# Optimization experiments

Hardware: AMD Instinct MI355X
Metric: run time of the kernel (lower is better)

Reference implementation:

```python
import jax, jax.numpy as jnp
import numpy as np
import math

V, D, H, F, L = 32000, 1024, 16, 4096, 6
B, S_DEC, S_ENC = 8, 512, 512
EPS = 1e-5


def _pos_encoding(seq_len, d_model):
    pos = jnp.arange(seq_len, dtype=jnp.float32)[:, None]
    div = jnp.exp(jnp.arange(0, d_model, 2, dtype=jnp.float32) * (-math.log(10000.0) / d_model))
    pe = jnp.zeros((seq_len, d_model), dtype=jnp.float32)
    pe = pe.at[:, 0::2].set(jnp.sin(pos * div))
    pe = pe.at[:, 1::2].set(jnp.cos(pos * div))
    return pe


def _layernorm(x, g, b):
    m = jnp.mean(x, axis=-1, keepdims=True)
    v = jnp.mean((x - m) ** 2, axis=-1, keepdims=True)
    return (x - m) * jax.lax.rsqrt(v + EPS) * g + b


def _mha(q_in, k_in, v_in, w, b, mask, n_heads):
    # w: [4, D, D] stored as [in, out] (q,k,v,o); b: [4, D]
    bsz, sq, dm = q_in.shape
    hd = dm // n_heads
    q = (q_in @ w[0] + b[0]).reshape(bsz, sq, n_heads, hd)
    k = (k_in @ w[1] + b[1]).reshape(bsz, -1, n_heads, hd)
    v = (v_in @ w[2] + b[2]).reshape(bsz, -1, n_heads, hd)
    scores = jnp.einsum('bqhd,bkhd->bhqk', q, k) / jnp.sqrt(jnp.asarray(hd, q.dtype))
    if mask is not None:
        scores = jnp.where(mask, jnp.asarray(-1e15, scores.dtype), scores)
    att = jax.nn.softmax(scores, axis=-1)
    out = jnp.einsum('bhqk,bkhd->bqhd', att, v).reshape(bsz, sq, dm)
    return out @ w[3] + b[3]


def setup_inputs() -> dict:
    key = jax.random.key(0)
    ks = jax.random.split(key, 16)
    sc = 0.02
    enc_out = jax.random.normal(ks[0], (B, S_ENC, D), dtype=jnp.float32)
    dec_in = jax.random.randint(ks[1], (B, S_DEC), 0, V, dtype=jnp.int64)
    # no padding on encoder side
    enc_dec_mask = jnp.zeros((1, 1, S_DEC, S_ENC), dtype=bool)
    # causal mask: True above the diagonal -> masked out
    fut_mask = jnp.triu(jnp.ones((S_DEC, S_DEC), dtype=bool), k=1)[None, None]
    return {
        'encoder_output': enc_out,
        'decoder_input': dec_in,
        'encoder_decoder_mask': enc_dec_mask,
        'decoder_future_mask': fut_mask,
        'embed_table': jax.random.normal(ks[2], (V, D), dtype=jnp.float32) * sc,
        'sa_w': jax.random.normal(ks[3], (L, 4, D, D), dtype=jnp.float32) * sc,
        'sa_b': jnp.zeros((L, 4, D), dtype=jnp.float32),
        'ca_w': jax.random.normal(ks[4], (L, 4, D, D), dtype=jnp.float32) * sc,
        'ca_b': jnp.zeros((L, 4, D), dtype=jnp.float32),
        'ffn_w1': jax.random.normal(ks[5], (L, D, F), dtype=jnp.float32) * sc,
        'ffn_b1': jnp.zeros((L, F), dtype=jnp.float32),
        'ffn_w2': jax.random.normal(ks[6], (L, F, D), dtype=jnp.float32) * sc,
        'ffn_b2': jnp.zeros((L, D), dtype=jnp.float32),
        'ln_g': jnp.ones((L, 3, D), dtype=jnp.float32),
        'ln_b': jnp.zeros((L, 3, D), dtype=jnp.float32),
        'final_g': jnp.ones((D,), dtype=jnp.float32),
        'final_b': jnp.zeros((D,), dtype=jnp.float32),
    }


def reference(encoder_output, decoder_input, encoder_decoder_mask, decoder_future_mask,
              embed_table, sa_w, sa_b, ca_w, ca_b, ffn_w1, ffn_b1, ffn_w2, ffn_b2,
              ln_g, ln_b, final_g, final_b):
    seq_len = decoder_input.shape[1]
    x = embed_table[decoder_input] * jnp.asarray(math.sqrt(D), jnp.float32)
    x = x + _pos_encoding(seq_len, D)
    for l in range(L):
        # pre-norm self-attention (dropout is identity at eval)
        h = _layernorm(x, ln_g[l, 0], ln_b[l, 0])
        x = x + _mha(h, h, h, sa_w[l], sa_b[l], decoder_future_mask, H)
        # pre-norm cross-attention
        h = _layernorm(x, ln_g[l, 1], ln_b[l, 1])
        x = x + _mha(h, encoder_output, encoder_output, ca_w[l], ca_b[l], encoder_decoder_mask, H)
        # pre-norm FFN
        h = _layernorm(x, ln_g[l, 2], ln_b[l, 2])
        x = x + jax.nn.relu(h @ ffn_w1[l] + ffn_b1[l]) @ ffn_w2[l] + ffn_b2[l]
    return _layernorm(x, final_g, final_b)
```

## Files before the change

### kernel.cpp

```cpp
#include <hip/hip_runtime.h>
#include <hip/hip_bf16.h>

typedef __attribute__((ext_vector_type(8))) short bf16x8;
typedef __attribute__((ext_vector_type(4))) float f32x4;
typedef __hip_bfloat16 bf16;

constexpr int DM   = 1024;
constexpr int NH   = 16;
constexpr int HD   = 64;
constexpr int FF   = 4096;
constexpr int NL   = 6;
constexpr int NB_  = 8;
constexpr int SEQL = 512;
constexpr int NTOK = NB_ * SEQL;

__device__ __forceinline__ void gl_lds16(const void* g, void* l) {
  __builtin_amdgcn_global_load_lds(
      (const __attribute__((address_space(1))) unsigned int*)g,
      (__attribute__((address_space(3))) unsigned int*)l, 16, 0, 0);
}

__global__ __launch_bounds__(256) void transpose_cvt(const float* __restrict__ src,
                                                     bf16* __restrict__ dst,
                                                     int R, int C) {
  __shared__ float tile[32][33];
  size_t mo = (size_t)blockIdx.z * R * C;
  src += mo; dst += mo;
  int c0 = blockIdx.x * 32, r0 = blockIdx.y * 32;
  int tx = threadIdx.x, ty = threadIdx.y;
  #pragma unroll
  for (int j = 0; j < 4; ++j)
    tile[ty + 8*j][tx] = src[(size_t)(r0 + ty + 8*j) * C + c0 + tx];
  __syncthreads();
  #pragma unroll
  for (int j = 0; j < 4; ++j)
    dst[(size_t)(c0 + ty + 8*j) * R + r0 + tx] = __float2bfloat16(tile[tx][ty + 8*j]);
}

__global__ __launch_bounds__(256) void cvt_bf16(const float* __restrict__ s,
                                                bf16* __restrict__ d) {
  size_t i = (size_t)blockIdx.x * 256 + threadIdx.x;
  float4 v = ((const float4*)s)[i];
  union { bf16 h[4]; uint2 u; } t;
  t.h[0] = __float2bfloat16(v.x); t.h[1] = __float2bfloat16(v.y);
  t.h[2] = __float2bfloat16(v.z); t.h[3] = __float2bfloat16(v.w);
  *(uint2*)(d + i * 4) = t.u;
}

__global__ __launch_bounds__(256) void vtrans(const bf16* __restrict__ in,
                                              bf16* __restrict__ out) {
  __shared__ bf16 tile[32][33];
  int t0 = blockIdx.x * 32, d0 = blockIdx.y * 32;
  int tx = threadIdx.x, ty = threadIdx.y;
  #pragma unroll
  for (int j = 0; j < 4; ++j)
    tile[ty + 8*j][tx] = in[(size_t)(t0 + ty + 8*j) * 3072 + 2048 + d0 + tx];
  __syncthreads();
  #pragma unroll
  for (int j = 0; j < 4; ++j)
    out[(size_t)(d0 + ty + 8*j) * NTOK + t0 + tx] = tile[tx][ty + 8*j];
}

__global__ __launch_bounds__(256) void embed_pe(const int* __restrict__ tok,
                                                const float* __restrict__ table,
                                                float* __restrict__ x) {
  int t = blockIdx.x;
  int s = t & (SEQL - 1);
  int tk = tok[t];
  int d = threadIdx.x * 4;
  float4 e = *(const float4*)(table + (size_t)tk * DM + d);
  float o[4] = {e.x, e.y, e.z, e.w};
  const float NEGC = -9.210340371976184f / 1024.0f;
  #pragma unroll
  for (int i = 0; i < 4; ++i) {
    int dd = d + i;
    float div = __expf((float)(dd & ~1) * NEGC);
    float arg = (float)s * div;
    float pe = (dd & 1) ? cosf(arg) : sinf(arg);
    o[i] = o[i] * 32.0f + pe;
  }
  float4 ov = {o[0], o[1], o[2], o[3]};
  *(float4*)(x + (size_t)t * DM + d) = ov;
}

__device__ __forceinline__ void ln_wave(float4 v[4], const float* __restrict__ g,
                                        const float* __restrict__ bb,
                                        int row, int lane, bf16* ob, float* of, int outf32) {
  float s = 0.0f;
  #pragma unroll
  for (int i = 0; i < 4; ++i) s += v[i].x + v[i].y + v[i].z + v[i].w;
  #pragma unroll
  for (int o = 32; o; o >>= 1) s += __shfl_xor(s, o);
  float mean = s * (1.0f / DM);
  float s2 = 0.0f;
  #pragma unroll
  for (int i = 0; i < 4; ++i) {
    v[i].x -= mean; v[i].y -= mean; v[i].z -= mean; v[i].w -= mean;
    s2 += v[i].x*v[i].x + v[i].y*v[i].y + v[i].z*v[i].z + v[i].w*v[i].w;
  }
  #pragma unroll
  for (int o = 32; o; o >>= 1) s2 += __shfl_xor(s2, o);
  float rs = rsqrtf(s2 * (1.0f / DM) + 1e-5f);
  #pragma unroll
  for (int i = 0; i < 4; ++i) {
    int c = (lane + i * 64) * 4;
    float4 gg = *(const float4*)(g + c);
    float4 bv = *(const float4*)(bb + c);
    float y0 = v[i].x * rs * gg.x + bv.x;
    float y1 = v[i].y * rs * gg.y + bv.y;
    float y2 = v[i].z * rs * gg.z + bv.z;
    float y3 = v[i].w * rs * gg.w + bv.w;
    if (outf32) {
      float4 ov = {y0, y1, y2, y3};
      *(float4*)(of + (size_t)row * DM + c) = ov;
    } else {
      union { bf16 h[4]; uint2 u; } t;
      t.h[0] = __float2bfloat16(y0); t.h[1] = __float2bfloat16(y1);
      t.h[2] = __float2bfloat16(y2); t.h[3] = __float2bfloat16(y3);
      *(uint2*)(ob + (size_t)row * DM + c) = t.u;
    }
  }
}

template<int OUTF32>
__global__ __launch_bounds__(256) void ln_kernel(const float* __restrict__ x,
                                                 const float* __restrict__ g,
                                                 const float* __restrict__ bb,
                                                 bf16* __restrict__ ob,
                                                 float* __restrict__ of) {
  int wv = threadIdx.x >> 6, lane = threadIdx.x & 63;
  int row = blockIdx.x * 4 + wv;
  const float4* xr = (const float4*)(x + (size_t)row * DM);
  float4 v[4];
  #pragma unroll
  for (int i = 0; i < 4; ++i) v[i] = xr[lane + i * 64];
  ln_wave(v, g, bb, row, lane, ob, of, OUTF32);
}

template<int OUTF32>
__global__ __launch_bounds__(256) void ln_fused4(float* __restrict__ x,
                                                 const float* __restrict__ p,
                                                 const float* __restrict__ bias,
                                                 const float* __restrict__ g,
                                                 const float* __restrict__ bb,
                                                 bf16* __restrict__ ob,
                                                 float* __restrict__ of) {
  int wv = threadIdx.x >> 6, lane = threadIdx.x & 63;
  int row = blockIdx.x * 4 + wv;
  size_t rb = (size_t)row * DM;
  const size_t NM = (size_t)NTOK * DM;
  float4 v[4];
  #pragma unroll
  for (int i = 0; i < 4; ++i) {
    int c = (lane + i * 64) * 4;
    float4 xv = *(const float4*)(x + rb + c);
    float4 a0 = *(const float4*)(p + rb + c);
    float4 a1 = *(const float4*)(p + NM + rb + c);
    float4 a2 = *(const float4*)(p + 2*NM + rb + c);
    float4 a3 = *(const float4*)(p + 3*NM + rb + c);
    float4 bv = *(const float4*)(bias + c);
    xv.x += a0.x + a1.x + a2.x + a3.x + bv.x;
    xv.y += a0.y + a1.y + a2.y + a3.y + bv.y;
    xv.z += a0.z + a1.z + a2.z + a3.z + bv.z;
    xv.w += a0.w + a1.w + a2.w + a3.w + bv.w;
    *(float4*)(x + rb + c) = xv;
    v[i] = xv;
  }
  ln_wave(v, g, bb, row, lane, ob, of, OUTF32);
}

template<int EPI>
__global__ __launch_bounds__(256) void gemm_bt(const bf16* __restrict__ A,
                                               const bf16* __restrict__ Bt,
                                               const float* __restrict__ bias,
                                               bf16* __restrict__ Cb,
                                               float* __restrict__ Cf,
                                               int M, int N, int K) {
  constexpr int BN = 64, NFR = 2;
  __shared__ bf16 As[3][128 * 32];
  __shared__ bf16 Bs[3][BN * 32];
  int tid = threadIdx.x;
  int wave = tid >> 6, lane = tid & 63;
  int l4 = lane & 15, lhi = lane >> 4;
  int wr = wave >> 1, wc = wave & 1;
  int nwg = gridDim.x * gridDim.y;
  int bid = blockIdx.y * gridDim.x + blockIdx.x;
  int cpx = nwg >> 3;
  int swz = (bid & 7) * cpx + (bid >> 3);
  int bx = swz % gridDim.x, by = swz / gridDim.x;
  int brow = by * 128, bcol = bx * BN;
  f32x4 acc[4][NFR] = {};
  int srow = lane >> 2;
  int scol = (lane & 3) * 8;
  int T = K >> 5;

  auto stage = [&](int buf, int t) {
    int k0 = t * 32;
    #pragma unroll
    for (int i = 0; i < 2; ++i) {
      int rb = i * 64 + wave * 16;
      gl_lds16(A + (size_t)(brow + rb + srow) * K + k0 + scol, &As[buf][rb * 32]);
    }
    int rb = wave * 16;
    gl_lds16(Bt + (size_t)(bcol + rb + srow) * K + k0 + scol, &Bs[buf][rb * 32]);
  };
  auto compute = [&](int buf) {
    bf16x8 af[4], bfv[NFR];
    #pragma unroll
    for (int m = 0; m < 4; ++m)
      af[m] = *(const bf16x8*)&As[buf][(wr * 64 + m * 16 + l4) * 32 + lhi * 8];
    #pragma unroll
    for (int n = 0; n < NFR; ++n)
      bfv[n] = *(const bf16x8*)&Bs[buf][(wc * 32 + n * 16 + l4) * 32 + lhi * 8];
    #pragma unroll
    for (int m = 0; m < 4; ++m)
      #pragma unroll
      for (int n = 0; n < NFR; ++n)
        acc[m][n] = __builtin_amdgcn_mfma_f32_16x16x32_bf16(af[m], bfv[n], acc[m][n], 0, 0, 0);
  };

  stage(0, 0);
  stage(1, 1);
  for (int t = 0; t < T; ++t) {
    if (t < T - 1) asm volatile("s_waitcnt vmcnt(3)" ::: "memory");
    else           asm volatile("s_waitcnt vmcnt(0)" ::: "memory");
    __builtin_amdgcn_s_barrier();
    asm volatile("" ::: "memory");
    if (t + 2 < T) stage((t + 2) % 3, t + 2);
    compute(t % 3);
  }

  #pragma unroll
  for (int m = 0; m < 4; ++m) {
    int row0 = brow + wr * 64 + m * 16 + lhi * 4;
    #pragma unroll
    for (int n = 0; n < NFR; ++n) {
      int col = bcol + wc * 32 + n * 16 + l4;
      #pragma unroll
      for (int r = 0; r < 4; ++r) {
        int row = row0 + r;
        float v = acc[m][n][r];
        if (EPI == 0) {
          v += bias[col];
          Cb[(size_t)row * N + col] = __float2bfloat16(v);
        } else {
          v += bias[col];
          size_t idx = (size_t)row * N + col;
          Cf[idx] = Cf[idx] + v;
        }
      }
    }
  }
}

template<int EPI>
__global__ __launch_bounds__(512, 2) void gemm8x(const bf16* __restrict__ A,
                                                 const bf16* __restrict__ Bt,
                                                 const float* __restrict__ bias,
                                                 bf16* __restrict__ Cb,
                                                 float* __restrict__ Cf,
                                                 int M, int N, int K) {
  __shared__ bf16 S[8][8192];
  int tid = threadIdx.x;
  int wave = tid >> 6, lane = tid & 63;
  int l4 = lane & 15, lhi = lane >> 4;
  int wr = wave >> 2, wc = wave & 3;
  int nwg = gridDim.x * gridDim.y;
  int bid = blockIdx.y * gridDim.x + blockIdx.x;
  int cpx = nwg >> 3;
  int swz = (bid & 7) * cpx + (bid >> 3);
  int bx = swz % gridDim.x, by = swz / gridDim.x;
  int brow = by * 256, bcol = bx * 256;
  f32x4 acc[8][4] = {};

  int kbase = 0, Keff = K;
  if (EPI == 4) { Keff = K >> 2; kbase = blockIdx.z * Keff; }
  int T = Keff >> 6;

  int srcRow = tid >> 3;
  int srcKb  = ((tid & 7) << 4) ^ (((tid >> 5) & 1) << 5) ^ (((tid >> 4) & 1) << 6);
  int swzr   = (((l4 >> 2) & 1) << 4) ^ (((l4 >> 1) & 1) << 5);

  auto stageA = [&](int d, int half, int kt) {
    #pragma unroll
    for (int j = 0; j < 2; ++j) {
      int r = brow + half * 128 + j * 64 + srcRow;
      if (EPI == 6) r = ((r >> 10) << 12) + 2048 + (r & 1023);
      const char* src = (const char*)(A + (size_t)r * K + kbase + kt * 64) + srcKb;
      gl_lds16(src, (char*)&S[d * 2 + half][0] + j * 8192 + wave * 1024);
    }
  };
  auto stageB = [&](int d, int half, int kt) {
    #pragma unroll
    for (int j = 0; j < 2; ++j) {
      int r = bcol + half * 128 + j * 64 + srcRow;
      if (EPI == 5) r = ((r >> 10) << 12) + 1024 + (r & 1023);
      const char* src = (const char*)(Bt + (size_t)r * K + kbase + kt * 64) + srcKb;
      gl_lds16(src, (char*)&S[4 + d * 2 + half][0] + j * 8192 + wave * 1024);
    }
  };

  stageA(0, 0, 0); stageA(0, 1, 0); stageB(0, 0, 0); stageB(0, 1, 0);

  for (int i = 0; i < T; ++i) {
    int d = i & 1, od = d ^ 1;
    asm volatile("s_waitcnt vmcnt(0)" ::: "memory");
    __builtin_amdgcn_s_barrier();
    asm volatile("" ::: "memory");
    const bf16* As_ = &S[d * 2 + wr][0];
    const bf16* Bs_ = &S[4 + d * 2 + (wc >> 1)][0];
    int rB = (wc & 1) * 64;
    bool st = (i + 1) < T;

    bf16x8 bfv[4][2];
    #pragma unroll
    for (int n = 0; n < 4; ++n) {
      int r = rB + n * 16 + l4;
      #pragma unroll
      for (int ks = 0; ks < 2; ++ks)
        bfv[n][ks] = *(const bf16x8*)&Bs_[r * 64 + ((ks * 32 + lhi * 8) ^ swzr)];
    }
    bf16x8 afA[2][2], afB[2][2];
    #pragma unroll
    for (int mm = 0; mm < 2; ++mm) {
      int r = (0 * 2 + mm) * 16 + l4;
      #pragma unroll
      for (int ks = 0; ks < 2; ++ks)
        afA[mm][ks] = *(const bf16x8*)&As_[r * 64 + ((ks * 32 + lhi * 8) ^ swzr)];
    }
    if (st) { stageA(od, 0, i + 1); stageA(od, 1, i + 1); }

    #pragma unroll
    for (int mm = 0; mm < 2; ++mm) {
      int r = (1 * 2 + mm) * 16 + l4;
      #pragma unroll
      for (int ks = 0; ks < 2; ++ks)
        afB[mm][ks] = *(const bf16x8*)&As_[r * 64 + ((ks * 32 + lhi * 8) ^ swzr)];
    }
    if (st) { stageB(od, 0, i + 1); stageB(od, 1, i + 1); }
    __builtin_amdgcn_s_setprio(1);
    #pragma unroll
    for (int mm = 0; mm < 2; ++mm)
      #pragma unroll
      for (int ks = 0; ks < 2; ++ks)
        #pragma unroll
        for (int n = 0; n < 4; ++n)
          acc[0 * 2 + mm][n] = __builtin_amdgcn_mfma_f32_16x16x32_bf16(afA[mm][ks], bfv[n][ks], acc[0 * 2 + mm][n], 0, 0, 0);
    __builtin_amdgcn_s_setprio(0);

    #pragma unroll
    for (int mm = 0; mm < 2; ++mm) {
      int r = (2 * 2 + mm) * 16 + l4;
      #pragma unroll
      for (int ks = 0; ks < 2; ++ks)
        afA[mm][ks] = *(const bf16x8*)&As_[r * 64 + ((ks * 32 + lhi * 8) ^ swzr)];
    }
    __builtin_amdgcn_s_setprio(1);
    #pragma unroll
    for (int mm = 0; mm < 2; ++mm)
      #pragma unroll
      for (int ks = 0; ks < 2; ++ks)
        #pragma unroll
        for (int n = 0; n < 4; ++n)
          acc[1 * 2 + mm][n] = __builtin_amdgcn_mfma_f32_16x16x32_bf16(afB[mm][ks], bfv[n][ks], acc[1 * 2 + mm][n], 0, 0, 0);
    __builtin_amdgcn_s_setprio(0);

    #pragma unroll
    for (int mm = 0; mm < 2; ++mm) {
      int r = (3 * 2 + mm) * 16 + l4;
      #pragma unroll
      for (int ks = 0; ks < 2; ++ks)
        afB[mm][ks] = *(const bf16x8*)&As_[r * 64 + ((ks * 32 + lhi * 8) ^ swzr)];
    }
    __builtin_amdgcn_s_setprio(1);
    #pragma unroll
    for (int mm = 0; mm < 2; ++mm)
      #pragma unroll
      for (int ks = 0; ks < 2; ++ks)
        #pragma unroll
        for (int n = 0; n < 4; ++n)
          acc[2 * 2 + mm][n] = __builtin_amdgcn_mfma_f32_16x16x32_bf16(afA[mm][ks], bfv[n][ks], acc[2 * 2 + mm][n], 0, 0, 0);
    __builtin_amdgcn_s_setprio(0);

    __builtin_amdgcn_s_setprio(1);
    #pragma unroll
    for (int mm = 0; mm < 2; ++mm)
      #pragma unroll
      for (int ks = 0; ks < 2; ++ks)
        #pragma unroll
        for (int n = 0; n < 4; ++n)
          acc[3 * 2 + mm][n] = __builtin_amdgcn_mfma_f32_16x16x32_bf16(afB[mm][ks], bfv[n][ks], acc[3 * 2 + mm][n], 0, 0, 0);
    __builtin_amdgcn_s_setprio(0);
    asm volatile("" ::: "memory");
  }

  #pragma unroll
  for (int m = 0; m < 8; ++m) {
    int row0 = brow + wr * 128 + m * 16 + lhi * 4;
    #pragma unroll
    for (int n = 0; n < 4; ++n) {
      int col = bcol + wc * 64 + n * 16 + l4;
      #pragma unroll
      for (int r = 0; r < 4; ++r) {
        int row = row0 + r;
        float v = acc[m][n][r];
        if (EPI == 0) {
          v += bias[col];
          Cb[(size_t)row * N + col] = __float2bfloat16(v);
        } else if (EPI == 1) {
          v += bias[col];
          v = fmaxf(v, 0.0f);
          Cb[(size_t)row * N + col] = __float2bfloat16(v);
        } else if (EPI == 4) {
          Cf[(size_t)blockIdx.z * ((size_t)M * N) + (size_t)row * N + col] = v;
        } else if (EPI == 5) {
          v += bias[((col >> 10) << 12) + 1024 + (col & 1023)];
          Cb[(size_t)row * N + col] = __float2bfloat16(v);
        } else {
          v += bias[((row >> 10) << 12) + 2048 + (row & 1023)];
          Cb[(size_t)row * N + col] = __float2bfloat16(v);
        }
      }
    }
  }
}

template<int CAUSAL>
__global__ __launch_bounds__(256, 2) void attn_kernel(const bf16* __restrict__ qg,
                                                      const bf16* __restrict__ kg,
                                                      const bf16* __restrict__ vtg,
                                                      bf16* __restrict__ og,
                                                      int qs, int ks) {
  __shared__ bf16 P[4][16][520];
  __shared__ bf16 KV[4096];
  int qblk = blockIdx.x;
  int bh = blockIdx.y;
  int b = bh >> 4, h = bh & 15;
  int wave = threadIdx.x >> 6, lane = threadIdx.x & 63;
  int l4 = lane & 15, lhi = lane >> 4;
  int qbase = qblk * 64 + wave * 16;
  const int qmax = CAUSAL ? (qbase + 15) : 0x7fffffff;
  const int tmaxb = CAUSAL ? qblk : 7;

  int srow8 = lane >> 3;
  int sbyte = ((lane & 7) * 16) ^ (srow8 << 4);
  int rdswz = (l4 & 7) << 4;

  bf16x8 qa[2];
  {
    size_t qrow = (size_t)(b * SEQL + qbase + l4);
    #pragma unroll
    for (int kk = 0; kk < 2; ++kk)
      qa[kk] = *(const bf16x8*)&qg[qrow * qs + h * HD + kk * 32 + lhi * 8];
  }

  f32x4 acc[32] = {};
  #pragma unroll
  for (int t = 0; t < 8; ++t) {
    if (t <= tmaxb) {
      #pragma unroll
      for (int j = 0; j < 2; ++j) {
        int row = (wave * 2 + j) * 8 + srow8;
        const char* src = (const char*)(kg + (size_t)(b * SEQL + t * 64 + row) * ks + h * HD) + sbyte;
        gl_lds16(src, (char*)&KV[0] + (wave * 2 + j) * 1024);
      }
      asm volatile("s_waitcnt vmcnt(0)" ::: "memory");
      __builtin_amdgcn_s_barrier();
      asm volatile("" ::: "memory");
      #pragma unroll
      for (int n = 0; n < 4; ++n) {
        int nk = t * 4 + n;
        if (!CAUSAL || nk * 16 <= qmax) {
          #pragma unroll
          for (int kk = 0; kk < 2; ++kk) {
            bf16x8 kf = *(const bf16x8*)((const char*)&KV[0] + (n * 16 + l4) * 128 + ((kk * 64 + lhi * 16) ^ rdswz));
            acc[nk] = __builtin_amdgcn_mfma_f32_16x16x32_bf16(qa[kk], kf, acc[nk], 0, 0, 0);
          }
        }
      }
      __builtin_amdgcn_s_barrier();
      asm volatile("" ::: "memory");
    }
  }

  int qloc = qbase + lhi * 4;
  #pragma unroll
  for (int r = 0; r < 4; ++r) {
    float mx = -3.0e38f;
    #pragma unroll
    for (int n = 0; n < 32; ++n) {
      float sv = acc[n][r] * 0.125f;
      if (CAUSAL && (n * 16 + l4 > qloc + r)) sv = -3.0e38f;
      acc[n][r] = sv;
      mx = fmaxf(mx, sv);
    }
    #pragma unroll
    for (int o = 1; o < 16; o <<= 1) mx = fmaxf(mx, __shfl_xor(mx, o));
    float sum = 0.0f;
    #pragma unroll
    for (int n = 0; n < 32; ++n) {
      float p;
      if (CAUSAL && n * 16 > qmax) p = 0.0f;
      else p = __expf(acc[n][r] - mx);
      acc[n][r] = p;
      sum += p;
    }
    #pragma unroll
    for (int o = 1; o < 16; o <<= 1) sum += __shfl_xor(sum, o);
    float rcp = 1.0f / sum;
    #pragma unroll
    for (int n = 0; n < 32; ++n)
      P[wave][lhi * 4 + r][n * 16 + l4] = __float2bfloat16(acc[n][r] * rcp);
  }
  __syncthreads();

  f32x4 oacc[4] = {};
  #pragma unroll
  for (int t = 0; t < 8; ++t) {
    if (t <= tmaxb) {
      #pragma unroll
      for (int j = 0; j < 2; ++j) {
        int row = (wave * 2 + j) * 8 + srow8;
        const char* src = (const char*)(vtg + (size_t)(h * HD + row) * NTOK + b * SEQL + t * 64) + sbyte;
        gl_lds16(src, (char*)&KV[0] + (wave * 2 + j) * 1024);
      }
      asm volatile("s_waitcnt vmcnt(0)" ::: "memory");
      __builtin_amdgcn_s_barrier();
      asm volatile("" ::: "memory");
      #pragma unroll
      for (int ksl = 0; ksl < 2; ++ksl) {
        int kslot = t * 2 + ksl;
        if (!CAUSAL || kslot * 32 <= qmax) {
          bf16x8 pa = *(const bf16x8*)&P[wave][l4][kslot * 32 + lhi * 8];
          #pragma unroll
          for (int nn = 0; nn < 4; ++nn) {
            bf16x8 vf = *(const bf16x8*)((const char*)&KV[0] + (nn * 16 + l4) * 128 + ((ksl * 64 + lhi * 16) ^ rdswz));
            oacc[nn] = __builtin_amdgcn_mfma_f32_16x16x32_bf16(pa, vf, oacc[nn], 0, 0, 0);
          }
        }
      }
      __builtin_amdgcn_s_barrier();
      asm volatile("" ::: "memory");
    }
  }

  size_t orow = (size_t)(b * SEQL + qbase + lhi * 4);
  #pragma unroll
  for (int n = 0; n < 4; ++n)
    #pragma unroll
    for (int r = 0; r < 4; ++r)
      og[(orow + r) * DM + h * HD + n * 16 + l4] = __float2bfloat16(oacc[n][r]);
}

extern "C" void kernel_launch(void* const* d_in, const int* in_sizes, int n_in,
                              void* d_out, int out_size, void* d_ws, size_t ws_size,
                              hipStream_t stream) {
  (void)in_sizes; (void)n_in; (void)out_size;
  const float* enc   = (const float*)d_in[0];
  const int*   toks  = (const int*)  d_in[1];
  const float* table = (const float*)d_in[4];
  const float* sa_w  = (const float*)d_in[5];
  const float* sa_b  = (const float*)d_in[6];
  const float* ca_w  = (const float*)d_in[7];
  const float* ca_b  = (const float*)d_in[8];
  const float* f1w   = (const float*)d_in[9];
  const float* f1b   = (const float*)d_in[10];
  const float* f2w   = (const float*)d_in[11];
  const float* f2b   = (const float*)d_in[12];
  const float* lng   = (const float*)d_in[13];
  const float* lnbp  = (const float*)d_in[14];
  const float* fg    = (const float*)d_in[15];
  const float* fbp   = (const float*)d_in[16];
  float* outp = (float*)d_out;

  char* base = (char*)d_ws;
  size_t off = 0;
  auto alloc = [&](size_t nbytes) -> char* {
    char* p = base + off;
    off += (nbytes + 255) & ~(size_t)255;
    return p;
  };
  const size_t DDb = (size_t)DM * DM;
  bf16* wt_sa   = (bf16*)alloc((size_t)NL * 4 * DDb * 2);
  bf16* wt_ca   = (bf16*)alloc((size_t)NL * 4 * DDb * 2);
  bf16* wt_f1   = (bf16*)alloc((size_t)NL * FF * DM * 2);
  bf16* wt_f2   = (bf16*)alloc((size_t)NL * FF * DM * 2);
  bf16* encb    = (bf16*)alloc((size_t)NTOK * DM * 2);
  bf16* keall   = (bf16*)alloc((size_t)NTOK * NL * DM * 2);
  bf16* vteall  = (bf16*)alloc((size_t)NL * DM * NTOK * 2);
  bf16* hbuf    = (bf16*)alloc((size_t)NTOK * DM * 2);
  bf16* qkvbuf  = (bf16*)alloc((size_t)NTOK * 3 * DM * 2);
  bf16* vtbuf   = (bf16*)alloc((size_t)NTOK * DM * 2);
  bf16* aobuf   = (bf16*)alloc((size_t)NTOK * DM * 2);
  bf16* h1buf   = (bf16*)alloc((size_t)NTOK * FF * 2);
  float* xbuf   = (float*)alloc((size_t)NTOK * DM * 4);
  float* pbuf4  = (float*)alloc((size_t)4 * NTOK * DM * 4);
  if (off > ws_size) return;

  dim3 tb(32, 8);
  transpose_cvt<<<dim3(DM/32, DM/32, NL*4), tb, 0, stream>>>(sa_w, wt_sa, DM, DM);
  transpose_cvt<<<dim3(DM/32, DM/32, NL*4), tb, 0, stream>>>(ca_w, wt_ca, DM, DM);
  transpose_cvt<<<dim3(FF/32, DM/32, NL),   tb, 0, stream>>>(f1w, wt_f1, DM, FF);
  transpose_cvt<<<dim3(DM/32, FF/32, NL),   tb, 0, stream>>>(f2w, wt_f2, FF, DM);
  cvt_bf16<<<(NTOK * DM / 4) / 256, 256, 0, stream>>>(enc, encb);
  embed_pe<<<NTOK, 256, 0, stream>>>(toks, table, xbuf);

  gemm8x<5><<<dim3(NL*DM/256, NTOK/256), 512, 0, stream>>>(encb, wt_ca, ca_b, keall, nullptr, NTOK, NL*DM, DM);
  gemm8x<6><<<dim3(NTOK/256, NL*DM/256), 512, 0, stream>>>(wt_ca, encb, ca_b, vteall, nullptr, NL*DM, NTOK, DM);

  ln_kernel<0><<<NTOK/4, 256, 0, stream>>>(xbuf, lng + 0*DM, lnbp + 0*DM, hbuf, nullptr);

  for (int l = 0; l < NL; ++l) {
    const bf16* wsa = wt_sa + (size_t)l * 4 * DDb;
    const bf16* wca = wt_ca + (size_t)l * 4 * DDb;
    const float* bsa = sa_b + (size_t)l * 4 * DM;
    const float* bca = ca_b + (size_t)l * 4 * DM;
    gemm8x<0><<<dim3(3*DM/256, NTOK/256), 512, 0, stream>>>(hbuf, wsa, bsa, qkvbuf, nullptr, NTOK, 3*DM, DM);
    vtrans<<<dim3(NTOK/32, DM/32), tb, 0, stream>>>(qkvbuf, vtbuf);
    attn_kernel<1><<<dim3(SEQL/64, NB_*NH), 256, 0, stream>>>(qkvbuf, qkvbuf + DM, vtbuf, aobuf, 3*DM, 3*DM);
    gemm_bt<3><<<dim3(DM/64, NTOK/128), 256, 0, stream>>>(aobuf, wsa + 3*DDb, bsa + 3*DM, nullptr, xbuf, NTOK, DM, DM);
    ln_kernel<0><<<NTOK/4, 256, 0, stream>>>(xbuf, lng + (l*3+1)*DM, lnbp + (l*3+1)*DM, hbuf, nullptr);
    gemm_bt<0><<<dim3(DM/64, NTOK/128), 256, 0, stream>>>(hbuf, wca + 0*DDb, bca + 0*DM, qkvbuf, nullptr, NTOK, DM, DM);
    attn_kernel<0><<<dim3(SEQL/64, NB_*NH), 256, 0, stream>>>(qkvbuf, keall + l*DM, vteall + (size_t)l*DM*NTOK, aobuf, DM, NL*DM);
    gemm_bt<3><<<dim3(DM/64, NTOK/128), 256, 0, stream>>>(aobuf, wca + 3*DDb, bca + 3*DM, nullptr, xbuf, NTOK, DM, DM);
    ln_kernel<0><<<NTOK/4, 256, 0, stream>>>(xbuf, lng + (l*3+2)*DM, lnbp + (l*3+2)*DM, hbuf, nullptr);
    gemm8x<1><<<dim3(FF/256, NTOK/256), 512, 0, stream>>>(hbuf, wt_f1 + (size_t)l*FF*DM, f1b + (size_t)l*FF, h1buf, nullptr, NTOK, FF, DM);
    gemm8x<4><<<dim3(DM/256, NTOK/256, 4), 512, 0, stream>>>(h1buf, wt_f2 + (size_t)l*FF*DM, nullptr, nullptr, pbuf4, NTOK, DM, FF);
    if (l < NL - 1)
      ln_fused4<0><<<NTOK/4, 256, 0, stream>>>(xbuf, pbuf4, f2b + (size_t)l*DM,
                                               lng + ((l+1)*3+0)*DM, lnbp + ((l+1)*3+0)*DM, hbuf, nullptr);
    else
      ln_fused4<1><<<NTOK/4, 256, 0, stream>>>(xbuf, pbuf4, f2b + (size_t)l*DM,
                                               fg, fbp, nullptr, outp);
  }
}
```

Baseline: 2.028 ms.

## Merge encoder K/V GEMMs into one launch, move residual add into LN, swizzle attention grid

The two encoder-side cross-attention K and V projection GEMMs now run in a single dual-role launch, sharing one grid instead of two back-to-back kernels. The o-projection GEMMs write plain fp32 partials, and a new fused LayerNorm kernel does the residual-plus-bias add, which removes the read-modify-write of x from the GEMM epilogue. The attention grid is remapped with an XCD-style block swizzle for better cache locality. In exchange, the fused LN reads an extra fp32 buffer, and the swizzle mapping assumes a fixed grid shape.

```diff
diff --git a/kernel.cpp b/kernel.cpp
--- a/kernel.cpp
+++ b/kernel.cpp
@@ -134,6 +134,34 @@
   float4 v[4];
   #pragma unroll
   for (int i = 0; i < 4; ++i) v[i] = xr[lane + i * 64];
+  ln_wave(v, g, bb, row, lane, ob, of, OUTF32);
+}
+
+template<int OUTF32>
+__global__ __launch_bounds__(256) void ln_fused1(float* __restrict__ x,
+                                                 const float* __restrict__ p,
+                                                 const float* __restrict__ bias,
+                                                 const float* __restrict__ g,
+                                                 const float* __restrict__ bb,
+                                                 bf16* __restrict__ ob,
+                                                 float* __restrict__ of) {
+  int wv = threadIdx.x >> 6, lane = threadIdx.x & 63;
+  int row = blockIdx.x * 4 + wv;
+  size_t rb = (size_t)row * DM;
+  float4 v[4];
+  #pragma unroll
+  for (int i = 0; i < 4; ++i) {
+    int c = (lane + i * 64) * 4;
+    float4 xv = *(const float4*)(x + rb + c);
+    float4 a0 = *(const float4*)(p + rb + c);
+    float4 bv = *(const float4*)(bias + c);
+    xv.x += a0.x + bv.x;
+    xv.y += a0.y + bv.y;
+    xv.z += a0.z + bv.z;
+    xv.w += a0.w + bv.w;
+    *(float4*)(x + rb + c) = xv;
+    v[i] = xv;
+  }
   ln_wave(v, g, bb, row, lane, ob, of, OUTF32);
 }
 
@@ -243,10 +271,12 @@
         if (EPI == 0) {
           v += bias[col];
           Cb[(size_t)row * N + col] = __float2bfloat16(v);
-        } else {
+        } else if (EPI == 3) {
           v += bias[col];
           size_t idx = (size_t)row * N + col;
           Cf[idx] = Cf[idx] + v;
+        } else {
+          Cf[(size_t)row * N + col] = v;
         }
       }
     }
@@ -254,27 +284,23 @@
 }
 
 template<int EPI>
-__global__ __launch_bounds__(512, 2) void gemm8x(const bf16* __restrict__ A,
-                                                 const bf16* __restrict__ Bt,
-                                                 const float* __restrict__ bias,
-                                                 bf16* __restrict__ Cb,
-                                                 float* __restrict__ Cf,
-                                                 int M, int N, int K) {
-  __shared__ bf16 S[8][8192];
+__device__ __forceinline__ void gemm8x_body(bf16 (*S)[8192],
+                                            const bf16* __restrict__ A,
+                                            const bf16* __restrict__ Bt,
+                                            const float* __restrict__ bias,
+                                            bf16* __restrict__ Cb,
+                                            float* __restrict__ Cf,
+                                            int M, int N, int K,
+                                            int bx, int by, int kz) {
   int tid = threadIdx.x;
   int wave = tid >> 6, lane = tid & 63;
   int l4 = lane & 15, lhi = lane >> 4;
   int wr = wave >> 2, wc = wave & 3;
-  int nwg = gridDim.x * gridDim.y;
-  int bid = blockIdx.y * gridDim.x + blockIdx.x;
-  int cpx = nwg >> 3;
-  int swz = (bid & 7) * cpx + (bid >> 3);
-  int bx = swz % gridDim.x, by = swz / gridDim.x;
   int brow = by * 256, bcol = bx * 256;
   f32x4 acc[8][4] = {};
 
   int kbase = 0, Keff = K;
-  if (EPI == 4) { Keff = K >> 2; kbase = blockIdx.z * Keff; }
+  if (EPI == 4) { Keff = K >> 2; kbase = kz * Keff; }
   int T = Keff >> 6;
 
   int srcRow = tid >> 3;
@@ -323,7 +349,7 @@
     bf16x8 afA[2][2], afB[2][2];
     #pragma unroll
     for (int mm = 0; mm < 2; ++mm) {
-      int r = (0 * 2 + mm) * 16 + l4;
+      int r = mm * 16 + l4;
       #pragma unroll
       for (int ks = 0; ks < 2; ++ks)
         afA[mm][ks] = *(const bf16x8*)&As_[r * 64 + ((ks * 32 + lhi * 8) ^ swzr)];
@@ -332,7 +358,7 @@
 
     #pragma unroll
     for (int mm = 0; mm < 2; ++mm) {
-      int r = (1 * 2 + mm) * 16 + l4;
+      int r = (2 + mm) * 16 + l4;
       #pragma unroll
       for (int ks = 0; ks < 2; ++ks)
         afB[mm][ks] = *(const bf16x8*)&As_[r * 64 + ((ks * 32 + lhi * 8) ^ swzr)];
@@ -345,12 +371,12 @@
       for (int ks = 0; ks < 2; ++ks)
         #pragma unroll
         for (int n = 0; n < 4; ++n)
-          acc[0 * 2 + mm][n] = __builtin_amdgcn_mfma_f32_16x16x32_bf16(afA[mm][ks], bfv[n][ks], acc[0 * 2 + mm][n], 0, 0, 0);
+          acc[mm][n] = __builtin_amdgcn_mfma_f32_16x16x32_bf16(afA[mm][ks], bfv[n][ks], acc[mm][n], 0, 0, 0);
     __builtin_amdgcn_s_setprio(0);
 
     #pragma unroll
     for (int mm = 0; mm < 2; ++mm) {
-      int r = (2 * 2 + mm) * 16 + l4;
+      int r = (4 + mm) * 16 + l4;
       #pragma unroll
       for (int ks = 0; ks < 2; ++ks)
         afA[mm][ks] = *(const bf16x8*)&As_[r * 64 + ((ks * 32 + lhi * 8) ^ swzr)];
@@ -362,12 +388,12 @@
       for (int ks = 0; ks < 2; ++ks)
         #pragma unroll
         for (int n = 0; n < 4; ++n)
-          acc[1 * 2 + mm][n] = __builtin_amdgcn_mfma_f32_16x16x32_bf16(afB[mm][ks], bfv[n][ks], acc[1 * 2 + mm][n], 0, 0, 0);
+          acc[2 + mm][n] = __builtin_amdgcn_mfma_f32_16x16x32_bf16(afB[mm][ks], bfv[n][ks], acc[2 + mm][n], 0, 0, 0);
     __builtin_amdgcn_s_setprio(0);
 
     #pragma unroll
     for (int mm = 0; mm < 2; ++mm) {
-      int r = (3 * 2 + mm) * 16 + l4;
+      int r = (6 + mm) * 16 + l4;
       #pragma unroll
       for (int ks = 0; ks < 2; ++ks)
         afB[mm][ks] = *(const bf16x8*)&As_[r * 64 + ((ks * 32 + lhi * 8) ^ swzr)];
@@ -379,7 +405,7 @@
       for (int ks = 0; ks < 2; ++ks)
         #pragma unroll
         for (int n = 0; n < 4; ++n)
-          acc[2 * 2 + mm][n] = __builtin_amdgcn_mfma_f32_16x16x32_bf16(afA[mm][ks], bfv[n][ks], acc[2 * 2 + mm][n], 0, 0, 0);
+          acc[4 + mm][n] = __builtin_amdgcn_mfma_f32_16x16x32_bf16(afA[mm][ks], bfv[n][ks], acc[4 + mm][n], 0, 0, 0);
     __builtin_amdgcn_s_setprio(0);
 
     __builtin_amdgcn_s_setprio(1);
@@ -389,7 +415,7 @@
       for (int ks = 0; ks < 2; ++ks)
         #pragma unroll
         for (int n = 0; n < 4; ++n)
-          acc[3 * 2 + mm][n] = __builtin_amdgcn_mfma_f32_16x16x32_bf16(afB[mm][ks], bfv[n][ks], acc[3 * 2 + mm][n], 0, 0, 0);
+          acc[6 + mm][n] = __builtin_amdgcn_mfma_f32_16x16x32_bf16(afB[mm][ks], bfv[n][ks], acc[6 + mm][n], 0, 0, 0);
     __builtin_amdgcn_s_setprio(0);
     asm volatile("" ::: "memory");
   }
@@ -412,7 +438,7 @@
           v = fmaxf(v, 0.0f);
           Cb[(size_t)row * N + col] = __float2bfloat16(v);
         } else if (EPI == 4) {
-          Cf[(size_t)blockIdx.z * ((size_t)M * N) + (size_t)row * N + col] = v;
+          Cf[(size_t)kz * ((size_t)M * N) + (size_t)row * N + col] = v;
         } else if (EPI == 5) {
           v += bias[((col >> 10) << 12) + 1024 + (col & 1023)];
           Cb[(size_t)row * N + col] = __float2bfloat16(v);
@@ -425,6 +451,41 @@
   }
 }
 
+template<int EPI>
+__global__ __launch_bounds__(512, 2) void gemm8x(const bf16* __restrict__ A,
+                                                 const bf16* __restrict__ Bt,
+                                                 const float* __restrict__ bias,
+                                                 bf16* __restrict__ Cb,
+                                                 float* __restrict__ Cf,
+                                                 int M, int N, int K) {
+  __shared__ bf16 S[8][8192];
+  int nwg = gridDim.x * gridDim.y;
+  int bid = blockIdx.y * gridDim.x + blockIdx.x;
+  int cpx = nwg >> 3;
+  int swz = (bid & 7) * cpx + (bid >> 3);
+  int bx = swz % gridDim.x, by = swz / gridDim.x;
+  gemm8x_body<EPI>(S, A, Bt, bias, Cb, Cf, M, N, K, bx, by, blockIdx.z);
+}
+
+__global__ __launch_bounds__(512, 2) void gemm8x_dual(const bf16* __restrict__ encb,
+                                                      const bf16* __restrict__ wca,
+                                                      const float* __restrict__ cab,
+                                                      bf16* __restrict__ keall,
+                                                      bf16* __restrict__ vteall) {
+  __shared__ bf16 S[8][8192];
+  int bid = blockIdx.x;
+  if (bid < 384) {
+    int swz = (bid & 7) * 48 + (bid >> 3);
+    int bx = swz % 24, by = swz / 24;
+    gemm8x_body<5>(S, encb, wca, cab, keall, nullptr, NTOK, NL*DM, DM, bx, by, 0);
+  } else {
+    int b2 = bid - 384;
+    int swz = (b2 & 7) * 48 + (b2 >> 3);
+    int bx = swz % 16, by = swz / 16;
+    gemm8x_body<6>(S, wca, encb, cab, vteall, nullptr, NL*DM, NTOK, DM, bx, by, 0);
+  }
+}
+
 template<int CAUSAL>
 __global__ __launch_bounds__(256, 2) void attn_kernel(const bf16* __restrict__ qg,
                                                       const bf16* __restrict__ kg,
@@ -433,8 +494,11 @@
                                                       int qs, int ks) {
   __shared__ bf16 P[4][16][520];
   __shared__ bf16 KV[4096];
-  int qblk = blockIdx.x;
-  int bh = blockIdx.y;
+  int nwg = gridDim.x * gridDim.y;
+  int lin = blockIdx.y * gridDim.x + blockIdx.x;
+  int swzb = (lin & 7) * (nwg >> 3) + (lin >> 3);
+  int qblk = swzb & 7;
+  int bh = swzb >> 3;
   int b = bh >> 4, h = bh & 15;
   int wave = threadIdx.x >> 6, lane = threadIdx.x & 63;
   int l4 = lane & 15, lhi = lane >> 4;
@@ -605,8 +669,7 @@
   cvt_bf16<<<(NTOK * DM / 4) / 256, 256, 0, stream>>>(enc, encb);
   embed_pe<<<NTOK, 256, 0, stream>>>(toks, table, xbuf);
 
-  gemm8x<5><<<dim3(NL*DM/256, NTOK/256), 512, 0, stream>>>(encb, wt_ca, ca_b, keall, nullptr, NTOK, NL*DM, DM);
-  gemm8x<6><<<dim3(NTOK/256, NL*DM/256), 512, 0, stream>>>(wt_ca, encb, ca_b, vteall, nullptr, NL*DM, NTOK, DM);
+  gemm8x_dual<<<768, 512, 0, stream>>>(encb, wt_ca, ca_b, keall, vteall);
 
   ln_kernel<0><<<NTOK/4, 256, 0, stream>>>(xbuf, lng + 0*DM, lnbp + 0*DM, hbuf, nullptr);
 
@@ -618,12 +681,14 @@
     gemm8x<0><<<dim3(3*DM/256, NTOK/256), 512, 0, stream>>>(hbuf, wsa, bsa, qkvbuf, nullptr, NTOK, 3*DM, DM);
     vtrans<<<dim3(NTOK/32, DM/32), tb, 0, stream>>>(qkvbuf, vtbuf);
     attn_kernel<1><<<dim3(SEQL/64, NB_*NH), 256, 0, stream>>>(qkvbuf, qkvbuf + DM, vtbuf, aobuf, 3*DM, 3*DM);
-    gemm_bt<3><<<dim3(DM/64, NTOK/128), 256, 0, stream>>>(aobuf, wsa + 3*DDb, bsa + 3*DM, nullptr, xbuf, NTOK, DM, DM);
-    ln_kernel<0><<<NTOK/4, 256, 0, stream>>>(xbuf, lng + (l*3+1)*DM, lnbp + (l*3+1)*DM, hbuf, nullptr);
+    gemm_bt<4><<<dim3(DM/64, NTOK/128), 256, 0, stream>>>(aobuf, wsa + 3*DDb, nullptr, nullptr, pbuf4, NTOK, DM, DM);
+    ln_fused1<0><<<NTOK/4, 256, 0, stream>>>(xbuf, pbuf4, bsa + 3*DM,
+                                             lng + (l*3+1)*DM, lnbp + (l*3+1)*DM, hbuf, nullptr);
     gemm_bt<0><<<dim3(DM/64, NTOK/128), 256, 0, stream>>>(hbuf, wca + 0*DDb, bca + 0*DM, qkvbuf, nullptr, NTOK, DM, DM);
     attn_kernel<0><<<dim3(SEQL/64, NB_*NH), 256, 0, stream>>>(qkvbuf, keall + l*DM, vteall + (size_t)l*DM*NTOK, aobuf, DM, NL*DM);
-    gemm_bt<3><<<dim3(DM/64, NTOK/128), 256, 0, stream>>>(aobuf, wca + 3*DDb, bca + 3*DM, nullptr, xbuf, NTOK, DM, DM);
-    ln_kernel<0><<<NTOK/4, 256, 0, stream>>>(xbuf, lng + (l*3+2)*DM, lnbp + (l*3+2)*DM, hbuf, nullptr);
+    gemm_bt<4><<<dim3(DM/64, NTOK/128), 256, 0, stream>>>(aobuf, wca + 3*DDb, nullptr, nullptr, pbuf4, NTOK, DM, DM);
+    ln_fused1<0><<<NTOK/4, 256, 0, stream>>>(xbuf, pbuf4, bca + 3*DM,
+                                             lng + (l*3+2)*DM, lnbp + (l*3+2)*DM, hbuf, nullptr);
     gemm8x<1><<<dim3(FF/256, NTOK/256), 512, 0, stream>>>(hbuf, wt_f1 + (size_t)l*FF*DM, f1b + (size_t)l*FF, h1buf, nullptr, NTOK, FF, DM);
     gemm8x<4><<<dim3(DM/256, NTOK/256, 4), 512, 0, stream>>>(h1buf, wt_f2 + (size_t)l*FF*DM, nullptr, nullptr, pbuf4, NTOK, DM, FF);
     if (l < NL - 1)
```

New measurement: 1.964 ms. 1.03x faster.
